# Kernel optimization log

Measured on AMD Instinct MI355X. Metric: run time of the kernel, lower is better.

## Reference

```python
import jax, jax.numpy as jnp
import numpy as np
from jax import lax

B, T, D, H, L = 128, 512, 256, 256, 2


def setup_inputs() -> dict:
    key = jax.random.key(0)
    ks = jax.random.split(key, 8)
    s = 1.0 / np.sqrt(H)
    return {
        "input1": jax.random.normal(ks[0], (B, T, D), jnp.float32),
        "input2": jax.random.normal(ks[1], (B, T, D), jnp.float32),
        "W_ih": jax.random.normal(ks[2], (L, 4 * H, D), jnp.float32) * s,
        "W_hh": jax.random.normal(ks[3], (L, 4 * H, H), jnp.float32) * s,
        "b_ih": jax.random.normal(ks[4], (L, 4 * H), jnp.float32) * s,
        "b_hh": jax.random.normal(ks[5], (L, 4 * H), jnp.float32) * s,
        "fc_w": jax.random.normal(ks[6], (5, H), jnp.float32) * s,
        "fc_b": jax.random.normal(ks[7], (5,), jnp.float32) * s,
    }


def _lstm_layer(x, Wih, Whh, bih, bhh):
    # x: [B, T, in]; returns (outputs [B, T, H], final h [B, H])
    b = x.shape[0]
    # precompute input projection for all timesteps (one big GEMM)
    xg = jnp.einsum('bti,gi->btg', x, Wih) + bih + bhh  # [B, T, 4H]
    h0 = jnp.zeros((b, H), x.dtype)
    c0 = jnp.zeros((b, H), x.dtype)

    def step(carry, xg_t):
        h, c = carry
        gates = xg_t + h @ Whh.T  # [B, 4H]
        i, f, g, o = jnp.split(gates, 4, axis=-1)
        i = jax.nn.sigmoid(i)
        f = jax.nn.sigmoid(f)
        g = jnp.tanh(g)
        o = jax.nn.sigmoid(o)
        c = f * c + i * g
        h = o * jnp.tanh(c)
        return (h, c), h

    (h_last, _), hs = lax.scan(step, (h0, c0), jnp.swapaxes(xg, 0, 1))
    return jnp.swapaxes(hs, 0, 1), h_last


def _forward_once(x, W_ih, W_hh, b_ih, b_hh, fc_w, fc_b):
    h_finals = []
    out = x
    for l in range(L):
        out, h_last = _lstm_layer(out, W_ih[l], W_hh[l], b_ih[l], b_hh[l])
        h_finals.append(h_last)
    hn = jnp.stack(h_finals, axis=0).reshape(-1, H)  # [L*B, H] (torch hn.view)
    return jax.nn.relu(hn) @ fc_w.T + fc_b  # [L*B, 5]


def reference(input1, input2, W_ih, W_hh, b_ih, b_hh, fc_w, fc_b):
    out1 = _forward_once(input1, W_ih, W_hh, b_ih, b_hh, fc_w, fc_b)
    out2 = _forward_once(input2, W_ih, W_hh, b_ih, b_hh, fc_w, fc_b)
    return (out1, out2)
```

## Files before the change

### kernel.cpp

```cpp
#include <hip/hip_runtime.h>
#include <hip/hip_fp16.h>

typedef unsigned int  u32;
typedef unsigned short u16;

typedef _Float16 h2v __attribute__((ext_vector_type(2)));
typedef _Float16 h4v __attribute__((ext_vector_type(4)));
typedef float    f4v __attribute__((ext_vector_type(4)));

static __device__ __forceinline__ u16 f2h_bits(float x){
    _Float16 h = (_Float16)x;
    return __builtin_bit_cast(u16, h);
}
static __device__ __forceinline__ u32 pack2(float a, float b){
    return (u32)f2h_bits(a) | ((u32)f2h_bits(b) << 16);
}
static __device__ __forceinline__ float fdot2(u32 w, u32 h, float acc){
#if __has_builtin(__builtin_amdgcn_fdot2)
    return __builtin_amdgcn_fdot2(__builtin_bit_cast(h2v, w),
                                  __builtin_bit_cast(h2v, h), acc, false);
#else
    h2v wv = __builtin_bit_cast(h2v, w), hv = __builtin_bit_cast(h2v, h);
    return acc + (float)wv[0]*(float)hv[0] + (float)wv[1]*(float)hv[1];
#endif
}
template<int CTRL>
static __device__ __forceinline__ float dpp_qp(float x){
#if __has_builtin(__builtin_amdgcn_mov_dpp)
    int r = __builtin_amdgcn_mov_dpp(__builtin_bit_cast(int, x), CTRL, 0xF, 0xF, true);
    return __builtin_bit_cast(float, r);
#else
    return __shfl_xor(x, (CTRL == 0xB1) ? 1 : 2);
#endif
}


__global__ void cvt_weights(const float* __restrict__ Wih,
                            const float* __restrict__ Whh,
                            const float* __restrict__ bih,
                            const float* __restrict__ bhh,
                            u32* __restrict__ wih16u,
                            u32* __restrict__ wreg,
                            u32* __restrict__ wldsg,
                            float* __restrict__ bias){
    u32 e = blockIdx.x * blockDim.x + threadIdx.x;
    {
        float2 v = ((const float2*)Wih)[e];
        wih16u[e] = pack2(v.x, v.y);
    }
    if (e < 196608u){
        u32 l = (e >= 98304u) ? 1u : 0u;
        u32 rem = e - l*98304u;
        u32 pidx = rem >> 10, L = rem & 1023u;
        u32 r = pidx / 24u, p = pidx - r*24u;
        u32 j = L >> 2, q = L & 3u;
        u32 row = r*256u + j;
        u32 P = 32u*q + p;
        float2 v = ((const float2*)Whh)[((size_t)l*1024u + row)*128u + P];
        wreg[e] = pack2(v.x, v.y);
    } else {
        u32 e2 = e - 196608u;
        u32 l = e2 >> 15, rem = e2 & 32767u;
        u32 i2 = rem >> 10, L = rem & 1023u;
        u32 r = i2 >> 3, k = i2 & 7u;
        u32 j = L >> 2, q = L & 3u;
        u32 row = r*256u + j;
        u32 P = 32u*q + 24u + k;
        float2 v = ((const float2*)Whh)[((size_t)l*1024u + row)*128u + P];
        wldsg[e2] = pack2(v.x, v.y);
    }
    if (e < 2048u){
        u32 l = e >> 10, Ls = e & 1023u;
        u32 src = l*1024u + (((Ls & 3u) << 8) | (Ls >> 2));
        bias[e] = bih[src] + bhh[src];
    }
}

template<int A_FP32>
__global__ __launch_bounds__(256) void proj_gemm(
        const float* __restrict__ in1, const float* __restrict__ in2,
        const u16*  __restrict__ A16,
        const u16*  __restrict__ Bw,
        u16*        __restrict__ Cout,
        int t0, int lgTc){
    __shared__ u16 Blds[128][260];
    const int tid = threadIdx.x;
    const int n0 = blockIdx.x * 128;
    const int m0 = blockIdx.y * 128;

    {
        const u32* src = (const u32*)Bw;
        #pragma unroll
        for (int i = 0; i < 64; i++){
            int idx = i*256 + tid;
            int r  = idx >> 7;
            int cu = idx & 127;
            u32 v = src[(size_t)(n0 + r)*128 + cu];
            *(u32*)&Blds[r][cu*2] = v;
        }
    }
    __syncthreads();

    const int l   = tid & 63;
    const int wid = tid >> 6;
    const int wm = (wid >> 1) * 64;
    const int wn = (wid & 1) * 64;
    const int lr = l & 15;
    const int lk = l >> 4;

    f4v acc[4][4] = {};

    const float* a32[4];
    const u16*   a16[4];
    #pragma unroll
    for (int f = 0; f < 4; f++){
        int m = m0 + wm + f*16 + lr;
        if (A_FP32){
            int beta = m >> lgTc;
            int tc   = m & ((1 << lgTc) - 1);
            const float* base = (beta < 128) ? in1 : in2;
            a32[f] = base + ((size_t)(beta & 127)*512 + (size_t)(t0 + tc))*256;
        } else {
            a16[f] = A16 + (size_t)m*256;
        }
    }

    for (int k0 = 0; k0 < 256; k0 += 16){
        uint2 a_[4], b_[4];
        #pragma unroll
        for (int f = 0; f < 4; f++){
            if (A_FP32){
                float4 v = *(const float4*)(a32[f] + k0 + lk*4);
                a_[f] = make_uint2(pack2(v.x, v.y), pack2(v.z, v.w));
            } else {
                a_[f] = *(const uint2*)(a16[f] + k0 + lk*4);
            }
        }
        #pragma unroll
        for (int f = 0; f < 4; f++)
            b_[f] = *(const uint2*)&Blds[wn + f*16 + lr][k0 + lk*4];
        #pragma unroll
        for (int fm = 0; fm < 4; fm++)
            #pragma unroll
            for (int fn = 0; fn < 4; fn++)
                acc[fm][fn] = __builtin_amdgcn_mfma_f32_16x16x16f16(
                    __builtin_bit_cast(h4v, a_[fm]),
                    __builtin_bit_cast(h4v, b_[fn]),
                    acc[fm][fn], 0, 0, 0);
    }

    #pragma unroll
    for (int fm = 0; fm < 4; fm++){
        #pragma unroll
        for (int i = 0; i < 4; i++){
            int m = m0 + wm + fm*16 + lk*4 + i;
            size_t rowoff = (size_t)m*1024;
            #pragma unroll
            for (int fn = 0; fn < 4; fn++){
                int n = n0 + wn + fn*16 + lr;
                int np = ((n & 255) << 2) | (n >> 8);
                Cout[rowoff + np] = f2h_bits(acc[fm][fn][i]);
            }
        }
    }
}

__global__ __launch_bounds__(1024, 4) void lstm_rec(
        const u16* __restrict__ xg,
        const u32* __restrict__ wreg,
        const u32* __restrict__ wldsg,
        const float* __restrict__ bias,
        u16* __restrict__ hseq,
        u16* __restrict__ h_state,
        float* __restrict__ c_state,
        int Tc, int write_seq, int first){
    __shared__ u32 wlds[1024*36];
    __shared__ alignas(16) u16 hbufF[2*288];

    const int L    = threadIdx.x;
    const int q    = L & 3;
    const int j    = L >> 2;
    const int beta = blockIdx.x;

    u32 w[96];
    #pragma unroll
    for (int t = 0; t < 96; t++)
        w[t] = wreg[(size_t)t*1024 + L];
    #pragma unroll
    for (int i = 0; i < 32; i++)
        wlds[L*36 + i] = wldsg[(size_t)i*1024 + L];

    const float bs = bias[L];
    float c = 0.f;
    u16 hb_last = 0;
    if (q == 0){
        u16 h0 = first ? (u16)0 : h_state[(size_t)beta*256 + j];
        hbufF[72*(j >> 6) + (j & 63)] = h0;
        hb_last = h0;
        if (!first) c = c_state[(size_t)beta*256 + j];
    }
    __syncthreads();

    const u16* xr = xg + (size_t)beta * Tc * 1024 + L;
    u16 xcur = xr[0];
    const uint4* wr = (const uint4*)&wlds[L*36];

    for (int tc = 0; tc < Tc; tc++){
        u16 xnext = (tc + 1 < Tc) ? xr[(size_t)(tc+1)*1024] : (u16)0;

        const uint4* hv = (const uint4*)&hbufF[(tc & 1)*288 + 72*q];
        float pA = 0.f, pB = 0.f, pC = 0.f, pD = 0.f;

        #pragma unroll
        for (int i = 0; i < 6; i++){
            uint4 hh = hv[i];
            pA = fdot2(w[   4*i+0], hh.x, pA); pA = fdot2(w[   4*i+1], hh.y, pA);
            pA = fdot2(w[   4*i+2], hh.z, pA); pA = fdot2(w[   4*i+3], hh.w, pA);
            pB = fdot2(w[24+4*i+0], hh.x, pB); pB = fdot2(w[24+4*i+1], hh.y, pB);
            pB = fdot2(w[24+4*i+2], hh.z, pB); pB = fdot2(w[24+4*i+3], hh.w, pB);
            pC = fdot2(w[48+4*i+0], hh.x, pC); pC = fdot2(w[48+4*i+1], hh.y, pC);
            pC = fdot2(w[48+4*i+2], hh.z, pC); pC = fdot2(w[48+4*i+3], hh.w, pC);
            pD = fdot2(w[72+4*i+0], hh.x, pD); pD = fdot2(w[72+4*i+1], hh.y, pD);
            pD = fdot2(w[72+4*i+2], hh.z, pD); pD = fdot2(w[72+4*i+3], hh.w, pD);
        }
        #pragma unroll
        for (int m = 0; m < 2; m++){
            uint4 hh = hv[6+m];
            uint4 wa = wr[0+m], wb = wr[2+m], wc = wr[4+m], wd = wr[6+m];
            pA = fdot2(wa.x, hh.x, pA); pA = fdot2(wa.y, hh.y, pA);
            pA = fdot2(wa.z, hh.z, pA); pA = fdot2(wa.w, hh.w, pA);
            pB = fdot2(wb.x, hh.x, pB); pB = fdot2(wb.y, hh.y, pB);
            pB = fdot2(wb.z, hh.z, pB); pB = fdot2(wb.w, hh.w, pB);
            pC = fdot2(wc.x, hh.x, pC); pC = fdot2(wc.y, hh.y, pC);
            pC = fdot2(wc.z, hh.z, pC); pC = fdot2(wc.w, hh.w, pC);
            pD = fdot2(wd.x, hh.x, pD); pD = fdot2(wd.y, hh.y, pD);
            pD = fdot2(wd.z, hh.z, pD); pD = fdot2(wd.w, hh.w, pD);
        }

        float k0_ = (q & 1) ? pB : pA;
        float k1_ = (q & 1) ? pD : pC;
        float s0_ = (q & 1) ? pA : pB;
        float s1_ = (q & 1) ? pC : pD;
        k0_ += dpp_qp<0xB1>(s0_);
        k1_ += dpp_qp<0xB1>(s1_);
        float kf = (q & 2) ? k1_ : k0_;
        float sf = (q & 2) ? k0_ : k1_;
        kf += dpp_qp<0x4E>(sf);

        float acc = kf + bs + (float)__builtin_bit_cast(_Float16, xcur);

        float targ = (q == 2) ? 2.f*acc : -acc;
        float e1 = __expf(targ);
        float rr = 1.f / (1.f + e1);
        float a  = (q == 2) ? 1.f - 2.f*rr : rr;

        float p1 = dpp_qp<0xB1>(a);
        float p2 = dpp_qp<0x4E>(a);
        float p3 = dpp_qp<0x4E>(p1);

        c = (q == 0) ? (p1*c + a*p2) : 0.f;
        float e2 = __expf(2.f*c);
        float th = 1.f - 2.f/(e2 + 1.f);
        float h  = p3 * th;
        u16 hb = f2h_bits(h);

        if (q == 0){
            hbufF[((tc & 1)^1)*288 + 72*(j >> 6) + (j & 63)] = hb;
            hb_last = hb;
            if (write_seq) hseq[((size_t)beta*Tc + tc)*256 + j] = hb;
        }
        xcur = xnext;
        __syncthreads();
    }

    if (q == 0){
        h_state[(size_t)beta*256 + j] = hb_last;
        c_state[(size_t)beta*256 + j] = c;
    }
}

__global__ void fc_out(const u16* __restrict__ hlast,
                       const float* __restrict__ fcw,
                       const float* __restrict__ fcb,
                       float* __restrict__ out){
    int r = blockIdx.x;
    int lane = threadIdx.x;
    int inp = r >> 8, rem = r & 255, l = rem >> 7, b = rem & 127;
    int beta = inp*128 + b;
    const u16* h = hlast + ((size_t)l*256 + beta)*256;

    int j0 = lane * 4;
    uint2 hb = *(const uint2*)(h + j0);
    h2v p0 = __builtin_bit_cast(h2v, hb.x), p1 = __builtin_bit_cast(h2v, hb.y);
    float hv0 = fmaxf((float)p0[0], 0.f);
    float hv1 = fmaxf((float)p0[1], 0.f);
    float hv2 = fmaxf((float)p1[0], 0.f);
    float hv3 = fmaxf((float)p1[1], 0.f);

    float acc[5];
    #pragma unroll
    for (int k = 0; k < 5; k++){
        float4 w = *(const float4*)(fcw + k*256 + j0);
        acc[k] = hv0*w.x + hv1*w.y + hv2*w.z + hv3*w.w;
    }
    #pragma unroll
    for (int k = 0; k < 5; k++)
        #pragma unroll
        for (int off = 32; off > 0; off >>= 1)
            acc[k] += __shfl_xor(acc[k], off);
    if (lane == 0){
        #pragma unroll
        for (int k = 0; k < 5; k++)
            out[(size_t)r*5 + k] = acc[k] + fcb[k];
    }
}

extern "C" void kernel_launch(void* const* d_in, const int* in_sizes, int n_in,
                              void* d_out, int out_size, void* d_ws, size_t ws_size,
                              hipStream_t stream) {
    const float* in1 = (const float*)d_in[0];
    const float* in2 = (const float*)d_in[1];
    const float* Wih = (const float*)d_in[2];
    const float* Whh = (const float*)d_in[3];
    const float* bih = (const float*)d_in[4];
    const float* bhh = (const float*)d_in[5];
    const float* fcw = (const float*)d_in[6];
    const float* fcb = (const float*)d_in[7];
    float* out = (float*)d_out;

    char* ws = (char*)d_ws;
    u16*   wih16   = (u16*)  (ws + 0x000000);
    u32*   wreg    = (u32*)  (ws + 0x100000);
    u32*   wldsg   = (u32*)  (ws + 0x1C0000);
    float* bias    = (float*)(ws + 0x200000);
    u16*   h_state = (u16*)  (ws + 0x202000);
    float* c_state = (float*)(ws + 0x242000);
    const size_t chunk_off = 0x300000;

    int Tc = 8;
    for (int cand = 512; cand >= 8; cand >>= 1){
        if (chunk_off + (size_t)cand * 655360ull <= ws_size){ Tc = cand; break; }
    }
    int lgTc = 31 - __builtin_clz((u32)Tc);
    u16* xgc = (u16*)(ws + chunk_off);
    u16* hsc = (u16*)(ws + chunk_off + (size_t)Tc * 524288ull);

    cvt_weights<<<1024, 256, 0, stream>>>(Wih, Whh, bih, bhh,
                                          (u32*)wih16, wreg, wldsg, bias);

    const int nch = 512 / Tc;
    dim3 pg(8, 2*Tc);
    for (int k = 0; k < nch; k++){
        int t0 = k * Tc;
        proj_gemm<1><<<pg, 256, 0, stream>>>(in1, in2, (const u16*)nullptr,
                                             wih16, xgc, t0, lgTc);
        lstm_rec<<<256, 1024, 0, stream>>>((const u16*)xgc, wreg, wldsg, bias,
                                           hsc, h_state, c_state,
                                           Tc, 1, k == 0);
        proj_gemm<0><<<pg, 256, 0, stream>>>((const float*)nullptr, (const float*)nullptr,
                                             (const u16*)hsc,
                                             wih16 + 262144, xgc, 0, lgTc);
        lstm_rec<<<256, 1024, 0, stream>>>((const u16*)xgc, wreg + 98304, wldsg + 32768,
                                           bias + 1024,
                                           (u16*)nullptr, h_state + 65536, c_state + 65536,
                                           Tc, 0, k == 0);
    }
    fc_out<<<512, 64, 0, stream>>>(h_state, fcw, fcb, out);
}
```

Measured before the change: 2.555 ms.

## Stage GEMM A tile in LDS with 16x16x32 MFMA; shift more Whh into registers

The projection GEMM now loads the whole A tile (converted to fp16) into LDS with wide vector loads and uses the 16x16x32 f16 MFMA, replacing per-iteration strided global loads of A. The recurrent kernel keeps 112 instead of 96 packed Whh words per thread in registers and halves the LDS-resident part, which cuts per-step LDS reads. The cost is more register pressure in a 1024-thread kernel with launch bounds of 4, a risk of spills, and extra LDS in the GEMM that may lower occupancy.

```diff
diff --git a/kernel.cpp b/kernel.cpp
--- a/kernel.cpp
+++ b/kernel.cpp
@@ -5,7 +5,7 @@
 typedef unsigned short u16;
 
 typedef _Float16 h2v __attribute__((ext_vector_type(2)));
-typedef _Float16 h4v __attribute__((ext_vector_type(4)));
+typedef _Float16 h8v __attribute__((ext_vector_type(8)));
 typedef float    f4v __attribute__((ext_vector_type(4)));
 
 static __device__ __forceinline__ u16 f2h_bits(float x){
@@ -34,6 +34,8 @@
 #endif
 }
 
+#define NRP 28
+#define NLP 4
 
 __global__ void cvt_weights(const float* __restrict__ Wih,
                             const float* __restrict__ Whh,
@@ -48,24 +50,25 @@
         float2 v = ((const float2*)Wih)[e];
         wih16u[e] = pack2(v.x, v.y);
     }
-    if (e < 196608u){
-        u32 l = (e >= 98304u) ? 1u : 0u;
-        u32 rem = e - l*98304u;
+    if (e < 229376u){
+        u32 l = (e >= 114688u) ? 1u : 0u;
+        u32 rem = e - l*114688u;
         u32 pidx = rem >> 10, L = rem & 1023u;
-        u32 r = pidx / 24u, p = pidx - r*24u;
+        u32 r = pidx / NRP, p = pidx - r*NRP;
         u32 j = L >> 2, q = L & 3u;
         u32 row = r*256u + j;
         u32 P = 32u*q + p;
         float2 v = ((const float2*)Whh)[((size_t)l*1024u + row)*128u + P];
         wreg[e] = pack2(v.x, v.y);
     } else {
-        u32 e2 = e - 196608u;
-        u32 l = e2 >> 15, rem = e2 & 32767u;
+        u32 e2 = e - 229376u;
+        u32 l = (e2 >= 16384u) ? 1u : 0u;
+        u32 rem = e2 - l*16384u;
         u32 i2 = rem >> 10, L = rem & 1023u;
-        u32 r = i2 >> 3, k = i2 & 7u;
+        u32 r = i2 >> 2, k = i2 & 3u;
         u32 j = L >> 2, q = L & 3u;
         u32 row = r*256u + j;
-        u32 P = 32u*q + 24u + k;
+        u32 P = 32u*q + NRP + k;
         float2 v = ((const float2*)Whh)[((size_t)l*1024u + row)*128u + P];
         wldsg[e2] = pack2(v.x, v.y);
     }
@@ -83,20 +86,42 @@
         const u16*  __restrict__ Bw,
         u16*        __restrict__ Cout,
         int t0, int lgTc){
-    __shared__ u16 Blds[128][260];
+    __shared__ u16 Alds[128][264];
+    __shared__ u16 Blds[128][264];
     const int tid = threadIdx.x;
     const int n0 = blockIdx.x * 128;
     const int m0 = blockIdx.y * 128;
 
     {
-        const u32* src = (const u32*)Bw;
-        #pragma unroll
-        for (int i = 0; i < 64; i++){
+        const uint4* src = (const uint4*)Bw;
+        #pragma unroll
+        for (int i = 0; i < 16; i++){
             int idx = i*256 + tid;
-            int r  = idx >> 7;
-            int cu = idx & 127;
-            u32 v = src[(size_t)(n0 + r)*128 + cu];
-            *(u32*)&Blds[r][cu*2] = v;
+            int r = idx >> 5, c4 = idx & 31;
+            uint4 v = src[(size_t)(n0 + r)*32 + c4];
+            *(uint4*)&Blds[r][c4*8] = v;
+        }
+    }
+    if (A_FP32){
+        #pragma unroll
+        for (int i = 0; i < 32; i++){
+            int idx = i*256 + tid;
+            int r = idx >> 6, c4 = idx & 63;
+            int m = m0 + r;
+            int beta = m >> lgTc;
+            int tc   = m & ((1 << lgTc) - 1);
+            const float* base = (beta < 128) ? in1 : in2;
+            float4 v = *(const float4*)(base + ((size_t)(beta & 127)*512 + (size_t)(t0 + tc))*256 + c4*4);
+            *(uint2*)&Alds[r][c4*4] = make_uint2(pack2(v.x, v.y), pack2(v.z, v.w));
+        }
+    } else {
+        const uint4* src = (const uint4*)A16;
+        #pragma unroll
+        for (int i = 0; i < 16; i++){
+            int idx = i*256 + tid;
+            int r = idx >> 5, c4 = idx & 31;
+            uint4 v = src[(size_t)(m0 + r)*32 + c4];
+            *(uint4*)&Alds[r][c4*8] = v;
         }
     }
     __syncthreads();
@@ -110,42 +135,23 @@
 
     f4v acc[4][4] = {};
 
-    const float* a32[4];
-    const u16*   a16[4];
-    #pragma unroll
-    for (int f = 0; f < 4; f++){
-        int m = m0 + wm + f*16 + lr;
-        if (A_FP32){
-            int beta = m >> lgTc;
-            int tc   = m & ((1 << lgTc) - 1);
-            const float* base = (beta < 128) ? in1 : in2;
-            a32[f] = base + ((size_t)(beta & 127)*512 + (size_t)(t0 + tc))*256;
-        } else {
-            a16[f] = A16 + (size_t)m*256;
-        }
-    }
-
-    for (int k0 = 0; k0 < 256; k0 += 16){
-        uint2 a_[4], b_[4];
-        #pragma unroll
-        for (int f = 0; f < 4; f++){
-            if (A_FP32){
-                float4 v = *(const float4*)(a32[f] + k0 + lk*4);
-                a_[f] = make_uint2(pack2(v.x, v.y), pack2(v.z, v.w));
-            } else {
-                a_[f] = *(const uint2*)(a16[f] + k0 + lk*4);
-            }
-        }
+    #pragma unroll
+    for (int ks = 0; ks < 8; ks++){
+        int k0 = ks*32 + lk*8;
+        uint4 a_[4], b_[4];
         #pragma unroll
         for (int f = 0; f < 4; f++)
-            b_[f] = *(const uint2*)&Blds[wn + f*16 + lr][k0 + lk*4];
+            a_[f] = *(const uint4*)&Alds[wm + f*16 + lr][k0];
+        #pragma unroll
+        for (int f = 0; f < 4; f++)
+            b_[f] = *(const uint4*)&Blds[wn + f*16 + lr][k0];
         #pragma unroll
         for (int fm = 0; fm < 4; fm++)
             #pragma unroll
             for (int fn = 0; fn < 4; fn++)
-                acc[fm][fn] = __builtin_amdgcn_mfma_f32_16x16x16f16(
-                    __builtin_bit_cast(h4v, a_[fm]),
-                    __builtin_bit_cast(h4v, b_[fn]),
+                acc[fm][fn] = __builtin_amdgcn_mfma_f32_16x16x32_f16(
+                    __builtin_bit_cast(h8v, a_[fm]),
+                    __builtin_bit_cast(h8v, b_[fn]),
                     acc[fm][fn], 0, 0, 0);
     }
 
@@ -174,7 +180,7 @@
         u16* __restrict__ h_state,
         float* __restrict__ c_state,
         int Tc, int write_seq, int first){
-    __shared__ u32 wlds[1024*36];
+    __shared__ u32 wlds[1024*20];
     __shared__ alignas(16) u16 hbufF[2*288];
 
     const int L    = threadIdx.x;
@@ -182,13 +188,13 @@
     const int j    = L >> 2;
     const int beta = blockIdx.x;
 
-    u32 w[96];
-    #pragma unroll
-    for (int t = 0; t < 96; t++)
+    u32 w[112];
+    #pragma unroll
+    for (int t = 0; t < 112; t++)
         w[t] = wreg[(size_t)t*1024 + L];
     #pragma unroll
-    for (int i = 0; i < 32; i++)
-        wlds[L*36 + i] = wldsg[(size_t)i*1024 + L];
+    for (int i = 0; i < 16; i++)
+        wlds[L*20 + i] = wldsg[(size_t)i*1024 + L];
 
     const float bs = bias[L];
     float c = 0.f;
@@ -203,7 +209,7 @@
 
     const u16* xr = xg + (size_t)beta * Tc * 1024 + L;
     u16 xcur = xr[0];
-    const uint4* wr = (const uint4*)&wlds[L*36];
+    const uint4* wr4 = (const uint4*)&wlds[L*20];
 
     for (int tc = 0; tc < Tc; tc++){
         u16 xnext = (tc + 1 < Tc) ? xr[(size_t)(tc+1)*1024] : (u16)0;
@@ -212,21 +218,20 @@
         float pA = 0.f, pB = 0.f, pC = 0.f, pD = 0.f;
 
         #pragma unroll
-        for (int i = 0; i < 6; i++){
+        for (int i = 0; i < 7; i++){
             uint4 hh = hv[i];
-            pA = fdot2(w[   4*i+0], hh.x, pA); pA = fdot2(w[   4*i+1], hh.y, pA);
-            pA = fdot2(w[   4*i+2], hh.z, pA); pA = fdot2(w[   4*i+3], hh.w, pA);
-            pB = fdot2(w[24+4*i+0], hh.x, pB); pB = fdot2(w[24+4*i+1], hh.y, pB);
-            pB = fdot2(w[24+4*i+2], hh.z, pB); pB = fdot2(w[24+4*i+3], hh.w, pB);
-            pC = fdot2(w[48+4*i+0], hh.x, pC); pC = fdot2(w[48+4*i+1], hh.y, pC);
-            pC = fdot2(w[48+4*i+2], hh.z, pC); pC = fdot2(w[48+4*i+3], hh.w, pC);
-            pD = fdot2(w[72+4*i+0], hh.x, pD); pD = fdot2(w[72+4*i+1], hh.y, pD);
-            pD = fdot2(w[72+4*i+2], hh.z, pD); pD = fdot2(w[72+4*i+3], hh.w, pD);
-        }
-        #pragma unroll
-        for (int m = 0; m < 2; m++){
-            uint4 hh = hv[6+m];
-            uint4 wa = wr[0+m], wb = wr[2+m], wc = wr[4+m], wd = wr[6+m];
+            pA = fdot2(w[    4*i+0], hh.x, pA); pA = fdot2(w[    4*i+1], hh.y, pA);
+            pA = fdot2(w[    4*i+2], hh.z, pA); pA = fdot2(w[    4*i+3], hh.w, pA);
+            pB = fdot2(w[28+ 4*i+0], hh.x, pB); pB = fdot2(w[28+ 4*i+1], hh.y, pB);
+            pB = fdot2(w[28+ 4*i+2], hh.z, pB); pB = fdot2(w[28+ 4*i+3], hh.w, pB);
+            pC = fdot2(w[56+ 4*i+0], hh.x, pC); pC = fdot2(w[56+ 4*i+1], hh.y, pC);
+            pC = fdot2(w[56+ 4*i+2], hh.z, pC); pC = fdot2(w[56+ 4*i+3], hh.w, pC);
+            pD = fdot2(w[84+ 4*i+0], hh.x, pD); pD = fdot2(w[84+ 4*i+1], hh.y, pD);
+            pD = fdot2(w[84+ 4*i+2], hh.z, pD); pD = fdot2(w[84+ 4*i+3], hh.w, pD);
+        }
+        {
+            uint4 hh = hv[7];
+            uint4 wa = wr4[0], wb = wr4[1], wc = wr4[2], wd = wr4[3];
             pA = fdot2(wa.x, hh.x, pA); pA = fdot2(wa.y, hh.y, pA);
             pA = fdot2(wa.z, hh.z, pA); pA = fdot2(wa.w, hh.w, pA);
             pB = fdot2(wb.x, hh.x, pB); pB = fdot2(wb.y, hh.y, pB);
@@ -331,7 +336,7 @@
     char* ws = (char*)d_ws;
     u16*   wih16   = (u16*)  (ws + 0x000000);
     u32*   wreg    = (u32*)  (ws + 0x100000);
-    u32*   wldsg   = (u32*)  (ws + 0x1C0000);
+    u32*   wldsg   = (u32*)  (ws + 0x1E0000);
     float* bias    = (float*)(ws + 0x200000);
     u16*   h_state = (u16*)  (ws + 0x202000);
     float* c_state = (float*)(ws + 0x242000);
@@ -360,7 +365,7 @@
         proj_gemm<0><<<pg, 256, 0, stream>>>((const float*)nullptr, (const float*)nullptr,
                                              (const u16*)hsc,
                                              wih16 + 262144, xgc, 0, lgTc);
-        lstm_rec<<<256, 1024, 0, stream>>>((const u16*)xgc, wreg + 98304, wldsg + 32768,
+        lstm_rec<<<256, 1024, 0, stream>>>((const u16*)xgc, wreg + 114688, wldsg + 16384,
                                            bias + 1024,
                                            (u16*)nullptr, h_state + 65536, c_state + 65536,
                                            Tc, 0, k == 0);
```

Result: slower. 2.923 ms (+14.4%).
